# Kernel tuning notes

Hardware: AMD Instinct MI355X
Metric: run time of the kernel (lower is better)

## Reference

```python
import jax, jax.numpy as jnp
import numpy as np


def setup_inputs() -> dict:
    key = jax.random.key(0)
    k1, k2 = jax.random.split(key)
    B, N, D = 32, 576, 1024  # CLIP ViT-L/14: 24x24 patches, width 1024
    hidden_states = jax.random.normal(k1, (B, N + 1, D), dtype=jnp.float32)
    cls_attn = jax.random.uniform(k2, (B, N), dtype=jnp.float32)
    return {"hidden_states": hidden_states, "cls_attn": cls_attn, "dominant_num": 128}


def scope_select(feats, cls_attn, num_selected):
    """Greedy coverage-maximizing token selection (SCOPE), batched.
    feats: [B, N, D], cls_attn: [B, N]. Returns selected indices [B, K].
    ALPHA=1.0 and COMBINED='multi' (the defaults in the source).
    """
    norm = feats / jnp.linalg.norm(feats, axis=-1, keepdims=True)
    sim = jnp.einsum('bnd,bmd->bnm', norm, norm)  # [B, N, N]
    B, N = feats.shape[0], feats.shape[1]
    batch_ix = jnp.arange(B)

    def step(carry, _):
        selected, cur_max = carry  # [B, N] bool, [B, N] float
        # zero out already-selected candidate columns j, then coverage gain
        masked = jnp.where(selected[:, None, :], 0.0, sim)  # [B, i, j]
        gains = jnp.maximum(masked - cur_max[:, :, None], 0.0).sum(axis=1)  # [B, N]
        gains = gains * cls_attn  # combined='multi', alpha=1.0
        gains = jnp.where(selected, -jnp.inf, gains)
        best = jnp.argmax(gains, axis=1)  # [B]
        selected = selected.at[batch_ix, best].set(True)
        cur_max = jnp.maximum(cur_max, sim[batch_ix, best])  # running coverage max
        return (selected, cur_max), best

    init = (jnp.zeros((B, N), dtype=bool), jnp.zeros((B, N), dtype=feats.dtype))
    _, idx = jax.lax.scan(step, init, None, length=num_selected)  # [K, B]
    return idx.T  # [B, K]


def reference(hidden_states, cls_attn, dominant_num):
    # drop CLS token (index 0) for selection
    image_features = hidden_states[:, 1:]  # [B, N, D]
    selected_idx = scope_select(image_features, cls_attn, dominant_num) + 1  # [B, K], +1 for CLS offset
    # torch masked_select preserves original index order -> gather sorted indices
    gather_idx = jnp.sort(selected_idx, axis=1)
    dominant_tokens = jnp.take_along_axis(hidden_states, gather_idx[:, :, None], axis=1)  # [B, K, D]
    return dominant_tokens, selected_idx
```

## Files before the change

kernel.cpp:

```cpp
#include <hip/hip_runtime.h>

#define BB 32
#define NN 576
#define DD 1024
#define KK 128
#define HS_N 577

typedef float v2f __attribute__((ext_vector_type(2)));

#define PKFMA_LO(ACC, A, B)                                                    \
    asm("v_pk_fma_f32 %0, %1, %2, %0 op_sel:[0,0,0] op_sel_hi:[0,1,1]"         \
        : "+v"(ACC) : "v"(A), "v"(B))
#define PKFMA_HI(ACC, A, B)                                                    \
    asm("v_pk_fma_f32 %0, %1, %2, %0 op_sel:[1,0,0] op_sel_hi:[1,1,1]"         \
        : "+v"(ACC) : "v"(A), "v"(B))

struct V2x2 { v2f lo, hi; };

__global__ __launch_bounds__(256) void norm_kernel(const float* __restrict__ hs,
                                                   float* __restrict__ inv) {
    int row = blockIdx.x;
    int b = row / NN, n = row % NN;
    const float4* p = (const float4*)(hs + ((size_t)b * HS_N + n + 1) * DD);
    int t = threadIdx.x;
    float4 v = p[t];
    double s = (double)v.x * v.x + (double)v.y * v.y + (double)v.z * v.z + (double)v.w * v.w;
    for (int off = 32; off; off >>= 1) s += __shfl_xor(s, off);
    __shared__ double wsum[4];
    int lane = t & 63, w = t >> 6;
    if (lane == 0) wsum[w] = s;
    __syncthreads();
    if (t == 0) {
        double tot = wsum[0] + wsum[1] + wsum[2] + wsum[3];
        inv[row] = 1.0f / (float)sqrt(tot);
    }
}

#define KC 32
#define LDT 68
#define TLD 68
__global__ __launch_bounds__(256) void sim_kernel(const float* __restrict__ hs,
                                                  const float* __restrict__ inv,
                                                  float* __restrict__ sim) {
    int id = blockIdx.x;
    int xcd = id & 7;
    int s = id >> 3;
    int b = xcd + 8 * (s / 45);
    int l = s % 45;
    int ti = 0;
    while (l >= 9 - ti) { l -= 9 - ti; ti++; }
    int tj = ti + l;
    int m0 = ti * 64, n0 = tj * 64;
    const float* feats = hs + ((size_t)b * HS_N + 1) * DD;
    __shared__ float smem[4][KC * LDT];
    float* tile = (float*)smem;
    int t = threadIdx.x;
    int lrow = t >> 2, lc8 = (t & 3) << 3;
    float invA = inv[b * NN + m0 + lrow];
    float invB = inv[b * NN + n0 + lrow];
    const float* gA = feats + (size_t)(m0 + lrow) * DD + lc8;
    const float* gB = feats + (size_t)(n0 + lrow) * DD + lc8;
    int tx = t & 15, ty = t >> 4;
    v2f acc2[4][2] = {};
    float4 a0 = *(const float4*)(gA);
    float4 a1 = *(const float4*)(gA + 4);
    float4 b0 = *(const float4*)(gB);
    float4 b1 = *(const float4*)(gB + 4);
    int cur = 0;
    for (int k0 = 0; k0 < DD; k0 += KC) {
        float* Ac = smem[cur];
        float* Bc = smem[2 + cur];
        Ac[(lc8 + 0) * LDT + lrow] = a0.x * invA;
        Ac[(lc8 + 1) * LDT + lrow] = a0.y * invA;
        Ac[(lc8 + 2) * LDT + lrow] = a0.z * invA;
        Ac[(lc8 + 3) * LDT + lrow] = a0.w * invA;
        Ac[(lc8 + 4) * LDT + lrow] = a1.x * invA;
        Ac[(lc8 + 5) * LDT + lrow] = a1.y * invA;
        Ac[(lc8 + 6) * LDT + lrow] = a1.z * invA;
        Ac[(lc8 + 7) * LDT + lrow] = a1.w * invA;
        Bc[(lc8 + 0) * LDT + lrow] = b0.x * invB;
        Bc[(lc8 + 1) * LDT + lrow] = b0.y * invB;
        Bc[(lc8 + 2) * LDT + lrow] = b0.z * invB;
        Bc[(lc8 + 3) * LDT + lrow] = b0.w * invB;
        Bc[(lc8 + 4) * LDT + lrow] = b1.x * invB;
        Bc[(lc8 + 5) * LDT + lrow] = b1.y * invB;
        Bc[(lc8 + 6) * LDT + lrow] = b1.z * invB;
        Bc[(lc8 + 7) * LDT + lrow] = b1.w * invB;
        __syncthreads();
        if (k0 + KC < DD) {
            a0 = *(const float4*)(gA + k0 + KC);
            a1 = *(const float4*)(gA + k0 + KC + 4);
            b0 = *(const float4*)(gB + k0 + KC);
            b1 = *(const float4*)(gB + k0 + KC + 4);
        }
#pragma unroll
        for (int kk = 0; kk < KC; kk++) {
            float4 av = *(const float4*)&Ac[kk * LDT + (tx << 2)];
            float4 bw = *(const float4*)&Bc[kk * LDT + (ty << 2)];
            V2x2 pa = __builtin_bit_cast(V2x2, av);
            V2x2 pb = __builtin_bit_cast(V2x2, bw);
            PKFMA_LO(acc2[0][0], pa.lo, pb.lo); PKFMA_LO(acc2[0][1], pa.lo, pb.hi);
            PKFMA_HI(acc2[1][0], pa.lo, pb.lo); PKFMA_HI(acc2[1][1], pa.lo, pb.hi);
            PKFMA_LO(acc2[2][0], pa.hi, pb.lo); PKFMA_LO(acc2[2][1], pa.hi, pb.hi);
            PKFMA_HI(acc2[3][0], pa.hi, pb.lo); PKFMA_HI(acc2[3][1], pa.hi, pb.hi);
        }
        cur ^= 1;
    }
#pragma unroll
    for (int i = 0; i < 4; i++) {
        size_t m = m0 + (tx << 2) + i;
        float4 o = {acc2[i][0][0], acc2[i][0][1], acc2[i][1][0], acc2[i][1][1]};
        *(float4*)(sim + ((size_t)b * NN + m) * NN + n0 + (ty << 2)) = o;
    }
    if (ti != tj) {
        __syncthreads();
#pragma unroll
        for (int i = 0; i < 4; i++) {
            float4 o = {acc2[i][0][0], acc2[i][0][1], acc2[i][1][0], acc2[i][1][1]};
            *(float4*)&tile[((tx << 2) + i) * TLD + (ty << 2)] = o;
        }
        __syncthreads();
#pragma unroll
        for (int r = 0; r < 4; r++) {
            int a = (tx << 2) + r;
            float4 o;
            o.x = tile[((ty << 2) + 0) * TLD + a];
            o.y = tile[((ty << 2) + 1) * TLD + a];
            o.z = tile[((ty << 2) + 2) * TLD + a];
            o.w = tile[((ty << 2) + 3) * TLD + a];
            *(float4*)(sim + ((size_t)b * NN + n0 + a) * NN + m0 + (ty << 2)) = o;
        }
    }
}

__global__ __launch_bounds__(256) void init_gain_kernel(const float* __restrict__ sim,
                                                        double* __restrict__ g0,
                                                        float* __restrict__ pad) {
    if (blockIdx.x == 0 && blockIdx.y == 0) {
        int tt = threadIdx.x;
        pad[tt] = 0.f; pad[tt + 256] = 0.f;
        if (tt < 64) pad[tt + 512] = 0.f;
    }
    int b = blockIdx.y;
    int m = (blockIdx.x << 2) + (threadIdx.x >> 6);
    int lane = threadIdx.x & 63;
    const float* row = sim + ((size_t)b * NN + m) * NN;
    double s = 0.0;
#pragma unroll
    for (int j = 0; j < 9; j++) s += (double)fmaxf(row[(j << 6) + lane], 0.f);
    for (int off = 32; off; off >>= 1) s += __shfl_xor(s, off);
    if (lane == 0) g0[b * NN + m] = s;
}

#define LOAD_BUF8(X, N4, J)                                                    \
    {                                                                          \
        int jj8 = (J) << 3;                                                    \
        int4 oa = *(const int4*)&choff[jj8];                                   \
        int4 ob = *(const int4*)&choff[jj8 + 4];                               \
        X[0] = *(const float*)(Sc + (unsigned)(oa.x + t4));                    \
        X[1] = *(const float*)(Sc + (unsigned)(oa.y + t4));                    \
        X[2] = *(const float*)(Sc + (unsigned)(oa.z + t4));                    \
        X[3] = *(const float*)(Sc + (unsigned)(oa.w + t4));                    \
        X[4] = *(const float*)(Sc + (unsigned)(ob.x + t4));                    \
        X[5] = *(const float*)(Sc + (unsigned)(ob.y + t4));                    \
        X[6] = *(const float*)(Sc + (unsigned)(ob.z + t4));                    \
        X[7] = *(const float*)(Sc + (unsigned)(ob.w + t4));                    \
        int jh = (J) << 2;                                                     \
        N4[0] = chonw4[jh + 0];                                                \
        N4[1] = chonw4[jh + 1];                                                \
        N4[2] = chonw4[jh + 2];                                                \
        N4[3] = chonw4[jh + 3];                                                \
    }

#define COMP_BUF8(X, N4)                                                       \
    {                                                                          \
        _Pragma("unroll") for (int q = 0; q < 4; q++) {                        \
            float o0 = N4[q].x, w0 = N4[q].y;                                  \
            gg += (double)(o0 - __builtin_amdgcn_fmed3f(X[2 * q], o0, w0));    \
            float o1 = N4[q].z, w1 = N4[q].w;                                  \
            gg += (double)(o1 - __builtin_amdgcn_fmed3f(X[2 * q + 1], o1, w1));\
        }                                                                      \
    }

__global__ __launch_bounds__(576, 1) void select_kernel(const float* __restrict__ sim,
                                                        const double* __restrict__ g0,
                                                        const float* __restrict__ cls,
                                                        float* __restrict__ out_idx,
                                                        int* __restrict__ gsorted) {
    int b = blockIdx.x;
    const float* S = sim + (size_t)b * NN * NN;
    const char* Sc = (const char*)S;
    int t = threadIdx.x, lane = t & 63, w = t >> 6;
    const int t4 = t << 2;
    __shared__ float2 ovnw[NN];
    __shared__ int    choff[NN + 8];
    __shared__ float4 chonw4[(NN + 8) / 2];
    __shared__ unsigned long long chmask[9];
    __shared__ double rv[9];
    __shared__ int    ri[9];
    __shared__ float  selseq[KK];
    __shared__ int    wcnt[9];
    float2* chonw = (float2*)chonw4;

    double gg = g0[b * NN + t];
    double cl = (double)cls[b * NN + t];
    float mycmax = 0.f;
    bool sel = false;
    const int c0 = t;

    for (int k = 0; k < KK; k++) {
        if (k > 0) {
            int pos = 0;
#pragma unroll
            for (int q = 0; q < 9; q++) {
                unsigned long long m = chmask[q];
                if ((m >> lane) & 1ull) {
                    int col = (q << 6) + lane;
                    int p = pos + __popcll(m & ((1ull << lane) - 1ull));
                    choff[p] = col * 2304;
                    chonw[p] = ovnw[col];
                }
                pos += __popcll(m);
            }
            int cc = pos;
            int padc = (8 - (cc & 7)) & 7;
            if (lane < padc) {
                choff[cc + lane] = NN * 2304;
                chonw[cc + lane] = make_float2(0.f, 0.f);
            }
            int nbat = (cc + padc) >> 3;

            float xA[8]; float4 nA[4];
            float xB[8]; float4 nB[4];
            float xC[8]; float4 nC[4];
            LOAD_BUF8(xA, nA, 0);
            if (nbat > 1) LOAD_BUF8(xB, nB, 1);
            for (int j = 0; j < nbat; ) {
                if (j + 2 < nbat) LOAD_BUF8(xC, nC, j + 2);
                __builtin_amdgcn_sched_barrier(0);
                COMP_BUF8(xA, nA);
                j++;
                if (j >= nbat) break;
                if (j + 2 < nbat) LOAD_BUF8(xA, nA, j + 2);
                __builtin_amdgcn_sched_barrier(0);
                COMP_BUF8(xB, nB);
                j++;
                if (j >= nbat) break;
                if (j + 2 < nbat) LOAD_BUF8(xB, nB, j + 2);
                __builtin_amdgcn_sched_barrier(0);
                COMP_BUF8(xC, nC);
                j++;
            }
        }
        double v = sel ? -1.0 : gg * cl;
        double vr = v;
        for (int off = 32; off; off >>= 1)
            vr = fmax(vr, __shfl_xor(vr, off));
        unsigned long long em = __ballot(v == vr);
        if (lane == 0) {
            rv[w] = vr;
            ri[w] = (w << 6) + (int)__builtin_ctzll(em);
        }
        __syncthreads();
        int risV[9];
#pragma unroll
        for (int q = 0; q < 9; q++) risV[q] = ri[q];
        float spec[9];
#pragma unroll
        for (int q = 0; q < 9; q++) spec[q] = S[(size_t)risV[q] * NN + t];
        double rvv[9];
#pragma unroll
        for (int q = 0; q < 9; q++) rvv[q] = rv[q];
        double m01 = fmax(rvv[0], rvv[1]), m23 = fmax(rvv[2], rvv[3]);
        double m45 = fmax(rvv[4], rvv[5]), m67 = fmax(rvv[6], rvv[7]);
        double m03 = fmax(m01, m23), m47 = fmax(m45, m67);
        double bv = fmax(fmax(m03, m47), rvv[8]);
        int mstar = risV[8]; float s0 = spec[8];
#pragma unroll
        for (int q = 8; q >= 0; q--) {
            bool hit = (rvv[q] == bv);
            mstar = hit ? risV[q] : mstar;
            s0 = hit ? spec[q] : s0;
        }
        float o0 = mycmax, n0 = fmaxf(o0, s0);
        bool h0 = n0 > o0;
        unsigned long long m0 = __ballot(h0);
        ovnw[c0] = make_float2(o0, n0); mycmax = n0;
        if (lane == 0) chmask[w] = m0;
        if (c0 == mstar) { sel = true; selseq[k] = (float)(mstar + 1); }
        __syncthreads();
    }

    if (t < KK) out_idx[b * KK + t] = selseq[t];
    unsigned long long mk = __ballot(sel);
    if (lane == 0) wcnt[w] = __popcll(mk);
    __syncthreads();
    int r = __popcll(mk & ((1ull << lane) - 1));
    int pre = 0;
#pragma unroll
    for (int q = 0; q < 9; q++) if (q < w) pre += wcnt[q];
    if (sel) gsorted[b * KK + pre + r] = c0 + 1;
}

__global__ __launch_bounds__(256) void gather_kernel(const float* __restrict__ hs,
                                                     const int* __restrict__ gsorted,
                                                     float* __restrict__ out) {
    int blk = blockIdx.x;
    int b = blk >> 7, j = blk & 127;
    int row = gsorted[b * KK + j];
    const float4* src = (const float4*)(hs + ((size_t)b * HS_N + row) * DD);
    float4* dst = (float4*)(out + ((size_t)b * KK + j) * DD);
    dst[threadIdx.x] = src[threadIdx.x];
}

extern "C" void kernel_launch(void* const* d_in, const int* in_sizes, int n_in,
                              void* d_out, int out_size, void* d_ws, size_t ws_size,
                              hipStream_t stream) {
    const float* hs = (const float*)d_in[0];
    const float* cls = (const float*)d_in[1];
    float* sim = (float*)d_ws;
    float* pad = sim + (size_t)BB * NN * NN;
    char* xregion = (char*)(pad + NN);
    float* inv = (float*)xregion;
    double* g0 = (double*)xregion;
    int* gsorted = (int*)(xregion + (size_t)BB * NN * sizeof(double));
    float* out_tokens = (float*)d_out;
    float* out_idx = out_tokens + (size_t)BB * KK * DD;

    norm_kernel<<<BB * NN, 256, 0, stream>>>(hs, inv);
    sim_kernel<<<45 * BB, 256, 0, stream>>>(hs, inv, sim);
    init_gain_kernel<<<dim3(NN / 4, BB), 256, 0, stream>>>(sim, g0, pad);
    select_kernel<<<BB, 576, 0, stream>>>(sim, g0, cls, out_idx, gsorted);
    gather_kernel<<<BB * KK, 256, 0, stream>>>(hs, gsorted, out_tokens);
}
```

Before: 626.4 us.

## Enlarge sim GEMM tiles to 96x96 with 6x6 per-thread micro-tiles

Rewrites the similarity kernel to use 96x96 output tiles (21 upper-triangle tile pairs per batch) with a 6x6 register micro-tile per thread instead of 64x64 tiles with 4x4 micro-tiles. This raises arithmetic intensity per shared-memory load and cuts the number of global reloads of the feature rows. In exchange it uses more registers, drops explicit double buffering in favour of two syncs per K step, and launches far fewer blocks (672), which may leave compute units underused.

```diff
diff --git a/kernel.cpp b/kernel.cpp
--- a/kernel.cpp
+++ b/kernel.cpp
@@ -36,99 +36,118 @@
     }
 }
 
-#define KC 32
-#define LDT 68
-#define TLD 68
+#define TS 96
+#define NTT 6
+#define NPAIR 21
+#define KC2 32
+#define LDK 196
+#define TLD2 100
 __global__ __launch_bounds__(256) void sim_kernel(const float* __restrict__ hs,
                                                   const float* __restrict__ inv,
                                                   float* __restrict__ sim) {
     int id = blockIdx.x;
     int xcd = id & 7;
     int s = id >> 3;
-    int b = xcd + 8 * (s / 45);
-    int l = s % 45;
+    int b = xcd + 8 * (s / NPAIR);
+    int l = s % NPAIR;
     int ti = 0;
-    while (l >= 9 - ti) { l -= 9 - ti; ti++; }
+    while (l >= NTT - ti) { l -= NTT - ti; ti++; }
     int tj = ti + l;
-    int m0 = ti * 64, n0 = tj * 64;
+    int m0 = ti * TS, n0 = tj * TS;
     const float* feats = hs + ((size_t)b * HS_N + 1) * DD;
-    __shared__ float smem[4][KC * LDT];
-    float* tile = (float*)smem;
+    __shared__ float smem[2 * KC2 * LDK];
+    float* As = smem;
+    float* Bs = smem + KC2 * LDK;
+    float* tile = smem;
     int t = threadIdx.x;
-    int lrow = t >> 2, lc8 = (t & 3) << 3;
-    float invA = inv[b * NN + m0 + lrow];
-    float invB = inv[b * NN + n0 + lrow];
-    const float* gA = feats + (size_t)(m0 + lrow) * DD + lc8;
-    const float* gB = feats + (size_t)(n0 + lrow) * DD + lc8;
+    int r0 = t >> 3, col4 = t & 7;
+    int sA[3]; float ivA[3], ivB[3];
+    const float* pA[3]; const float* pB[3];
+#pragma unroll
+    for (int q = 0; q < 3; q++) {
+        int r = r0 + 32 * q;
+        int slot = (r / 6) * 12 + (r % 6);
+        sA[q] = (col4 << 2) * LDK + slot;
+        ivA[q] = inv[b * NN + m0 + r];
+        ivB[q] = inv[b * NN + n0 + r];
+        pA[q] = feats + (size_t)(m0 + r) * DD + (col4 << 2);
+        pB[q] = feats + (size_t)(n0 + r) * DD + (col4 << 2);
+    }
     int tx = t & 15, ty = t >> 4;
-    v2f acc2[4][2] = {};
-    float4 a0 = *(const float4*)(gA);
-    float4 a1 = *(const float4*)(gA + 4);
-    float4 b0 = *(const float4*)(gB);
-    float4 b1 = *(const float4*)(gB + 4);
-    int cur = 0;
-    for (int k0 = 0; k0 < DD; k0 += KC) {
-        float* Ac = smem[cur];
-        float* Bc = smem[2 + cur];
-        Ac[(lc8 + 0) * LDT + lrow] = a0.x * invA;
-        Ac[(lc8 + 1) * LDT + lrow] = a0.y * invA;
-        Ac[(lc8 + 2) * LDT + lrow] = a0.z * invA;
-        Ac[(lc8 + 3) * LDT + lrow] = a0.w * invA;
-        Ac[(lc8 + 4) * LDT + lrow] = a1.x * invA;
-        Ac[(lc8 + 5) * LDT + lrow] = a1.y * invA;
-        Ac[(lc8 + 6) * LDT + lrow] = a1.z * invA;
-        Ac[(lc8 + 7) * LDT + lrow] = a1.w * invA;
-        Bc[(lc8 + 0) * LDT + lrow] = b0.x * invB;
-        Bc[(lc8 + 1) * LDT + lrow] = b0.y * invB;
-        Bc[(lc8 + 2) * LDT + lrow] = b0.z * invB;
-        Bc[(lc8 + 3) * LDT + lrow] = b0.w * invB;
-        Bc[(lc8 + 4) * LDT + lrow] = b1.x * invB;
-        Bc[(lc8 + 5) * LDT + lrow] = b1.y * invB;
-        Bc[(lc8 + 6) * LDT + lrow] = b1.z * invB;
-        Bc[(lc8 + 7) * LDT + lrow] = b1.w * invB;
-        __syncthreads();
-        if (k0 + KC < DD) {
-            a0 = *(const float4*)(gA + k0 + KC);
-            a1 = *(const float4*)(gA + k0 + KC + 4);
-            b0 = *(const float4*)(gB + k0 + KC);
-            b1 = *(const float4*)(gB + k0 + KC + 4);
-        }
-#pragma unroll
-        for (int kk = 0; kk < KC; kk++) {
-            float4 av = *(const float4*)&Ac[kk * LDT + (tx << 2)];
-            float4 bw = *(const float4*)&Bc[kk * LDT + (ty << 2)];
-            V2x2 pa = __builtin_bit_cast(V2x2, av);
-            V2x2 pb = __builtin_bit_cast(V2x2, bw);
-            PKFMA_LO(acc2[0][0], pa.lo, pb.lo); PKFMA_LO(acc2[0][1], pa.lo, pb.hi);
-            PKFMA_HI(acc2[1][0], pa.lo, pb.lo); PKFMA_HI(acc2[1][1], pa.lo, pb.hi);
-            PKFMA_LO(acc2[2][0], pa.hi, pb.lo); PKFMA_LO(acc2[2][1], pa.hi, pb.hi);
-            PKFMA_HI(acc2[3][0], pa.hi, pb.lo); PKFMA_HI(acc2[3][1], pa.hi, pb.hi);
-        }
-        cur ^= 1;
-    }
-#pragma unroll
-    for (int i = 0; i < 4; i++) {
-        size_t m = m0 + (tx << 2) + i;
-        float4 o = {acc2[i][0][0], acc2[i][0][1], acc2[i][1][0], acc2[i][1][1]};
-        *(float4*)(sim + ((size_t)b * NN + m) * NN + n0 + (ty << 2)) = o;
+    v2f acc[6][3] = {};
+    float4 va[3], vb[3];
+#pragma unroll
+    for (int q = 0; q < 3; q++) { va[q] = *(const float4*)(pA[q]); vb[q] = *(const float4*)(pB[q]); }
+    for (int k0 = 0; k0 < DD; k0 += KC2) {
+        __syncthreads();
+#pragma unroll
+        for (int q = 0; q < 3; q++) {
+            As[sA[q] + 0 * LDK] = va[q].x * ivA[q];
+            As[sA[q] + 1 * LDK] = va[q].y * ivA[q];
+            As[sA[q] + 2 * LDK] = va[q].z * ivA[q];
+            As[sA[q] + 3 * LDK] = va[q].w * ivA[q];
+            Bs[sA[q] + 0 * LDK] = vb[q].x * ivB[q];
+            Bs[sA[q] + 1 * LDK] = vb[q].y * ivB[q];
+            Bs[sA[q] + 2 * LDK] = vb[q].z * ivB[q];
+            Bs[sA[q] + 3 * LDK] = vb[q].w * ivB[q];
+        }
+        __syncthreads();
+        if (k0 + KC2 < DD) {
+#pragma unroll
+            for (int q = 0; q < 3; q++) {
+                va[q] = *(const float4*)(pA[q] + k0 + KC2);
+                vb[q] = *(const float4*)(pB[q] + k0 + KC2);
+            }
+        }
+#pragma unroll
+        for (int kk = 0; kk < KC2; kk++) {
+            const float* Ar = &As[kk * LDK + tx * 12];
+            const float* Br = &Bs[kk * LDK + ty * 12];
+            float4 a4 = *(const float4*)Ar;  float2 a2 = *(const float2*)(Ar + 4);
+            float4 b4 = *(const float4*)Br;  float2 b2 = *(const float2*)(Br + 4);
+            V2x2 paq = __builtin_bit_cast(V2x2, a4);
+            V2x2 pbq = __builtin_bit_cast(V2x2, b4);
+            v2f pa[3] = {paq.lo, paq.hi, __builtin_bit_cast(v2f, a2)};
+            v2f pb[3] = {pbq.lo, pbq.hi, __builtin_bit_cast(v2f, b2)};
+#pragma unroll
+            for (int ip = 0; ip < 3; ip++)
+#pragma unroll
+                for (int jp = 0; jp < 3; jp++) {
+                    PKFMA_LO(acc[2 * ip][jp], pa[ip], pb[jp]);
+                    PKFMA_HI(acc[2 * ip + 1][jp], pa[ip], pb[jp]);
+                }
+        }
+    }
+#pragma unroll
+    for (int i = 0; i < 6; i++) {
+        float* dst = sim + ((size_t)b * NN + m0 + tx * 6 + i) * NN + n0 + ty * 6;
+        *(float2*)(dst + 0) = make_float2(acc[i][0][0], acc[i][0][1]);
+        *(float2*)(dst + 2) = make_float2(acc[i][1][0], acc[i][1][1]);
+        *(float2*)(dst + 4) = make_float2(acc[i][2][0], acc[i][2][1]);
     }
     if (ti != tj) {
         __syncthreads();
 #pragma unroll
-        for (int i = 0; i < 4; i++) {
-            float4 o = {acc2[i][0][0], acc2[i][0][1], acc2[i][1][0], acc2[i][1][1]};
-            *(float4*)&tile[((tx << 2) + i) * TLD + (ty << 2)] = o;
-        }
-        __syncthreads();
-#pragma unroll
-        for (int r = 0; r < 4; r++) {
-            int a = (tx << 2) + r;
-            float4 o;
-            o.x = tile[((ty << 2) + 0) * TLD + a];
-            o.y = tile[((ty << 2) + 1) * TLD + a];
-            o.z = tile[((ty << 2) + 2) * TLD + a];
-            o.w = tile[((ty << 2) + 3) * TLD + a];
-            *(float4*)(sim + ((size_t)b * NN + n0 + a) * NN + m0 + (ty << 2)) = o;
+        for (int i = 0; i < 6; i++) {
+            float* d = &tile[(tx * 6 + i) * TLD2 + ty * 6];
+            *(float2*)(d + 0) = make_float2(acc[i][0][0], acc[i][0][1]);
+            *(float2*)(d + 2) = make_float2(acc[i][1][0], acc[i][1][1]);
+            *(float2*)(d + 4) = make_float2(acc[i][2][0], acc[i][2][1]);
+        }
+        __syncthreads();
+#pragma unroll
+        for (int i = 0; i < 6; i++) {
+            int a = tx * 6 + i;
+            float o0 = tile[(ty * 6 + 0) * TLD2 + a];
+            float o1 = tile[(ty * 6 + 1) * TLD2 + a];
+            float o2 = tile[(ty * 6 + 2) * TLD2 + a];
+            float o3 = tile[(ty * 6 + 3) * TLD2 + a];
+            float o4 = tile[(ty * 6 + 4) * TLD2 + a];
+            float o5 = tile[(ty * 6 + 5) * TLD2 + a];
+            float* dst = sim + ((size_t)b * NN + n0 + a) * NN + m0 + ty * 6;
+            *(float2*)(dst + 0) = make_float2(o0, o1);
+            *(float2*)(dst + 2) = make_float2(o2, o3);
+            *(float2*)(dst + 4) = make_float2(o4, o5);
         }
     }
 }
@@ -328,7 +347,7 @@
     float* out_idx = out_tokens + (size_t)BB * KK * DD;
 
     norm_kernel<<<BB * NN, 256, 0, stream>>>(hs, inv);
-    sim_kernel<<<45 * BB, 256, 0, stream>>>(hs, inv, sim);
+    sim_kernel<<<21 * BB, 256, 0, stream>>>(hs, inv, sim);
     init_gain_kernel<<<dim3(NN / 4, BB), 256, 0, stream>>>(sim, g0, pad);
     select_kernel<<<BB, 576, 0, stream>>>(sim, g0, cls, out_idx, gsorted);
     gather_kernel<<<BB * KK, 256, 0, stream>>>(hs, gsorted, out_tokens);
```

Result: slower. 643.6 us (+2.7%).
